# Kernel optimization log

Hardware: AMD Instinct MI355X
Metric: run time of the kernel (lower is better)

## Reference

```python
import jax, jax.numpy as jnp
import numpy as np

PAD = 9  # fixed padding from FNO1d.__init__


def setup_inputs() -> dict:
    key = jax.random.key(0)
    ks = jax.random.split(key, 12)
    B, N, F_IN = 64, 8192, 2          # batch, grid points, input features
    W, L, M = 64, 5, 16               # width, n fourier layers, modes
    d = {}
    d["x"] = jax.random.normal(ks[0], (B, N, F_IN), jnp.float32)
    # Lifting: Linear(F_IN -> W)
    d["lift_w"] = jax.random.normal(ks[1], (F_IN, W), jnp.float32) * 0.5
    d["lift_b"] = jnp.zeros((W,), jnp.float32)
    # Fourier kernels (complex, stored as real/imag), all layers W->W with M modes
    scale = 1.0 / (W * W)
    d["kern_r"] = jax.random.uniform(ks[2], (L, W, W, M), jnp.float32) * scale
    d["kern_i"] = jax.random.uniform(ks[3], (L, W, W, M), jnp.float32) * scale
    # 1x1 Conv1d skip per layer: weight (out, in), bias (out)
    d["conv_w"] = jax.random.normal(ks[4], (L, W, W), jnp.float32) * (1.0 / np.sqrt(W))
    d["conv_b"] = jnp.zeros((L, W), jnp.float32)
    # Projection: Linear(W -> 2W), GELU, Linear(2W -> 1)
    d["proj_w1"] = jax.random.normal(ks[5], (W, 2 * W), jnp.float32) * (1.0 / np.sqrt(W))
    d["proj_b1"] = jnp.zeros((2 * W,), jnp.float32)
    d["proj_w2"] = jax.random.normal(ks[6], (2 * W, 1), jnp.float32) * (1.0 / np.sqrt(2 * W))
    d["proj_b2"] = jnp.zeros((1,), jnp.float32)
    return d


def _fourier_layer(v, kern, cw, cb, modes):
    # v: (b, d, n) real. kern: (d_in, d_out, modes) complex.
    n = v.shape[-1]
    nyq = n // 2 + 1
    F = jnp.fft.rfft(v, axis=-1)                              # (b, d, nyq) complex
    Pm = jnp.einsum('bik,iok->bok', F[:, :, :modes], kern)    # (b, d_out, modes)
    P = jnp.pad(Pm, ((0, 0), (0, 0), (0, nyq - modes)))       # zero high freqs
    K = jnp.fft.irfft(P, n=n, axis=-1)                        # (b, d_out, n)
    lin = jnp.einsum('oi,bin->bon', cw, v) + cb[None, :, None]
    return lin + K


def reference(x, lift_w, lift_b, kern_r, kern_i, conv_w, conv_b,
              proj_w1, proj_b1, proj_w2, proj_b2):
    gelu = lambda t: jax.nn.gelu(t, approximate=False)  # torch.nn.GELU default is exact
    v = x @ lift_w + lift_b                    # (B, N, W)
    v = jnp.transpose(v, (0, 2, 1))            # (B, W, N)
    v = jnp.pad(v, ((0, 0), (0, 0), (0, PAD))) # (B, W, N+PAD)
    L = kern_r.shape[0]
    M = kern_r.shape[-1]
    for l in range(L):  # fixed small layer count
        kern = kern_r[l] + 1j * kern_i[l]
        v = gelu(_fourier_layer(v, kern, conv_w[l], conv_b[l], M))
    v = v[..., :-PAD]
    v = jnp.transpose(v, (0, 2, 1))            # (B, N, W)
    h = gelu(v @ proj_w1 + proj_b1)            # (B, N, 2W)
    return h @ proj_w2 + proj_b2               # (B, N, 1)
```

## Files before the change

kernel.cpp:

```cpp
#include <hip/hip_runtime.h>
#include <math.h>

#define NLEN 8201
#define NB 64
#define W 64
#define M 16
#define NL 5
#define TWO_PI 6.283185307179586476925286766559
#define NT_STAT 514
#define NSTEPS 257
#define NBLK 33

typedef unsigned short u16;
typedef __attribute__((ext_vector_type(8))) short bf16x8;
typedef __attribute__((ext_vector_type(4))) float f32x4;
typedef __attribute__((ext_vector_type(4))) short short4v;
typedef __attribute__((ext_vector_type(8))) short short8v;

__device__ __forceinline__ u16 bf16rn(float x) {
    unsigned u = __float_as_uint(x);
    unsigned r = (u + 0x7fffu + ((u >> 16) & 1u)) >> 16;
    return (u16)r;
}
__device__ __forceinline__ float bf16tof(u16 h) {
// ... 62 lines not shown
    int nstep = blockIdx.x;
    int t = threadIdx.x;
    for (int s = t; s < 1024; s += 256) {
        int e = s & 7, lane = (s >> 3) & 63, kcT = s >> 9;
        int kc = kcT * 16 + (lane & 15);
        int n = nstep * 32 + ((lane >> 4) << 3) + e;
        int k = kc & 15;
        long long m = ((long long)k * (long long)n) % NLEN;
        double th = (TWO_PI / (double)NLEN) * (double)m;
        double sv, cv;
        sincos(th, &sv, &cv);
        float val = (kc < 16) ? (float)cv : (float)(-sv);
        u16 h, lo;
        bf16split(val, h, lo);
        size_t base = (((size_t)nstep * 2 + kcT) * 2) * 512 + lane * 8 + e;
        Tdft[base] = h;
        Tdft[base + 512] = lo;
    }
}

__global__ __launch_bounds__(256) void kprep(const float* __restrict__ cw,
                                             u16* __restrict__ AcwBuf) {
    int l = blockIdx.x;
    int t = threadIdx.x;
    const float* cwl = cw + (size_t)l * W * W;
    u16* ob = AcwBuf + (size_t)l * 8192;
    for (int s = t; s < 4096; s += 256) {
        int e = s & 7, lane = (s >> 3) & 63, mt = (s >> 9) & 3, ks = s >> 11;
        int kk = ((lane >> 4) << 2) + (e & 3) + ((e >> 2) << 4);
        int k = ks * 32 + kk;
        int o = mt * 16 + (lane & 15);
        u16 h, lo;
        bf16split(cwl[o * 64 + k], h, lo);
        ob[(((size_t)ks * 2 + 0) * 4 + mt) * 512 + lane * 8 + e] = h;
        ob[(((size_t)ks * 2 + 1) * 4 + mt) * 512 + lane * 8 + e] = lo;
    }
}

__global__ __launch_bounds__(256) void kprep2(const float* __restrict__ w1,
                                              u16* __restrict__ Aw1) {
    int t = threadIdx.x;
    for (int s = t; s < 8192; s += 256) {
        int e = s & 7, lane = (s >> 3) & 63, mt = (s >> 9) & 7, ks = s >> 12;
        int kk = ((lane >> 4) << 2) + (e & 3) + ((e >> 2) << 4);
        int k = ks * 32 + kk;
        int h = mt * 16 + (lane & 15);
        u16 hh, lo;
        bf16split(w1[k * 128 + h], hh, lo);
        Aw1[(((size_t)ks * 2 + 0) * 8 + mt) * 512 + lane * 8 + e] = hh;
        Aw1[(((size_t)ks * 2 + 1) * 8 + mt) * 512 + lane * 8 + e] = lo;
    }
}

__device__ __forceinline__ void dft_tail(u16* lds, int wv, int lane, int t,
        int blk, const u16* __restrict__ Tdft, float* __restrict__ FpB,
        int atomicMode) {
    int nstep = blk * 8 + wv;
    if (nstep > NSTEPS - 1) nstep = NSTEPS - 1;
    const u16* at = Tdft + (size_t)nstep * 2048;
    bf16x8 Th0 = *(const bf16x8*)(at + lane * 8);
    bf16x8 Tl0 = *(const bf16x8*)(at + 512 + lane * 8);
    bf16x8 Th1 = *(const bf16x8*)(at + 1024 + lane * 8);
    bf16x8 Tl1 = *(const bf16x8*)(at + 1536 + lane * 8);
    f32x4 dacc[2][4];
    #pragma unroll
    for (int kt = 0; kt < 2; kt++)
        #pragma unroll
        for (int ot = 0; ot < 4; ot++) dacc[kt][ot] = (f32x4){0.f, 0.f, 0.f, 0.f};
    const u16* rd = lds + wv * 4096;
    int g = lane >> 4;
    #pragma unroll
    for (int ot = 0; ot < 4; ot++) {
        int oo = ot * 16 + (lane & 15);
        int swz = (oo & 7) << 4;
        bf16x8 Bh = *(const bf16x8*)(rd + (((oo * 128 + g * 16) ^ swz) >> 1));
        bf16x8 Bl = *(const bf16x8*)(rd + (((oo * 128 + 64 + g * 16) ^ swz) >> 1));
        dacc[0][ot] = __builtin_amdgcn_mfma_f32_16x16x32_bf16(Th0, Bh, dacc[0][ot], 0, 0, 0);
        dacc[0][ot] = __builtin_amdgcn_mfma_f32_16x16x32_bf16(Th0, Bl, dacc[0][ot], 0, 0, 0);
        dacc[0][ot] = __builtin_amdgcn_mfma_f32_16x16x32_bf16(Tl0, Bh, dacc[0][ot], 0, 0, 0);
        dacc[0][ot] = __builtin_amdgcn_mfma_f32_16x16x32_bf16(Tl0, Bl, dacc[0][ot], 0, 0, 0);
        dacc[1][ot] = __builtin_amdgcn_mfma_f32_16x16x32_bf16(Th1, Bh, dacc[1][ot], 0, 0, 0);
        dacc[1][ot] = __builtin_amdgcn_mfma_f32_16x16x32_bf16(Th1, Bl, dacc[1][ot], 0, 0, 0);
        dacc[1][ot] = __builtin_amdgcn_mfma_f32_16x16x32_bf16(Tl1, Bh, dacc[1][ot], 0, 0, 0);
        dacc[1][ot] = __builtin_amdgcn_mfma_f32_16x16x32_bf16(Tl1, Bl, dacc[1][ot], 0, 0, 0);
    }
    float* rw = (float*)lds + wv * 2048;
    #pragma unroll
    for (int kt = 0; kt < 2; kt++)
        #pragma unroll
        for (int ot = 0; ot < 4; ot++) {
            int oo = ot * 16 + (lane & 15);
            int kcb = kt * 16 + ((lane >> 4) << 2);
            rw[(kcb + 0) * 64 + oo] = dacc[kt][ot][0];
            rw[(kcb + 1) * 64 + oo] = dacc[kt][ot][1];
            rw[(kcb + 2) * 64 + oo] = dacc[kt][ot][2];
            rw[(kcb + 3) * 64 + oo] = dacc[kt][ot][3];
        }
    __syncthreads();
    {
        const float* rr = (const float*)lds;
        int idx = t * 4;
        float4 s = *(const float4*)(rr + idx);
        #pragma unroll
        for (int w2 = 1; w2 < 8; w2++) {
            float4 p = *(const float4*)(rr + w2 * 2048 + idx);
            s.x += p.x; s.y += p.y; s.z += p.z; s.w += p.w;
        }
        if (atomicMode) {
            atomicAddF(FpB + idx + 0, s.x);
            atomicAddF(FpB + idx + 1, s.y);
            atomicAddF(FpB + idx + 2, s.z);
            atomicAddF(FpB + idx + 3, s.w);
        } else {
            *(float4*)(FpB + (size_t)blk * 2048 + idx) = s;
        }
    }
}

__global__ __launch_bounds__(512, 4) void klift2(const float* __restrict__ x,
        const float* __restrict__ lw, const float* __restrict__ lb,
        u16* __restrict__ Vf, const u16* __restrict__ Tdft,
        float* __restrict__ Fpart, int fstride, int atomicMode) {
    __shared__ __align__(16) u16 outT[8 * 4096];
    int t = threadIdx.x;
    int b = blockIdx.y;
    int blk = blockIdx.x;
    int lane = t & 63;
    int wv = __builtin_amdgcn_readfirstlane(t >> 6);
    int r4 = (lane >> 4) << 2;
    u16* vfb = Vf + ((size_t)b * NBLK + blk) * 32768;
    int n0 = blk * 256;

    short4v hv[4][2], lv[4][2];
    #pragma unroll
    for (int ntl = 0; ntl < 2; ntl++) {
        int nt = wv * 2 + ntl;
        int n = n0 + nt * 16 + (lane & 15);
        float x0 = 0.f, x1 = 0.f;
        bool in = (n < 8192);
        if (in) {
            const float* xp = x + ((size_t)b * 8192 + n) * 2;
            x0 = xp[0]; x1 = xp[1];
        }
        #pragma unroll
        for (int mt = 0; mt < 4; mt++) {
            #pragma unroll
            for (int j = 0; j < 4; j++) {
                int o = mt * 16 + r4 + j;
                float val = in ? fmaf(x0, lw[o], fmaf(x1, lw[64 + o], lb[o])) : 0.f;
                u16 h, lo;
                bf16split(val, h, lo);
                hv[mt][ntl][j] = (short)h;
                lv[mt][ntl][j] = (short)lo;
            }
        }
        *(short8v*)(vfb + ((size_t)0 * 16 + nt) * 512 + lane * 8) = cat4(hv[0][ntl], hv[1][ntl]);
        *(short8v*)(vfb + ((size_t)1 * 16 + nt) * 512 + lane * 8) = cat4(lv[0][ntl], lv[1][ntl]);
        *(short8v*)(vfb + ((size_t)2 * 16 + nt) * 512 + lane * 8) = cat4(hv[2][ntl], hv[3][ntl]);
        *(short8v*)(vfb + ((size_t)3 * 16 + nt) * 512 + lane * 8) = cat4(lv[2][ntl], lv[3][ntl]);
    }

    u16* outW = outT + wv * 4096;
    #pragma unroll
    for (int ntl = 0; ntl < 2; ntl++) {
        int nl = ntl * 16 + (lane & 15);
        bool ok = (n0 + wv * 32 + nl) <= 8200;
        #pragma unroll
        for (int mt = 0; mt < 4; mt++) {
            #pragma unroll
            for (int j = 0; j < 4; j++) {
                int oo = mt * 16 + r4 + j;
                u16 h  = ok ? (u16)hv[mt][ntl][j] : (u16)0;
                u16 lo = ok ? (u16)lv[mt][ntl][j] : (u16)0;
                int raw = oo * 128 + nl * 2;
                int swz = (oo & 7) << 4;
                outW[(raw ^ swz) >> 1] = h;
                outW[((raw + 64) ^ swz) >> 1] = lo;
            }
        }
    }
    dft_tail(outT, wv, lane, t, blk, Tdft, Fpart + (size_t)b * fstride, atomicMode);
}

__device__ __forceinline__ void wfrag(u16* wb2, int mt, int kk, int ol, float val) {
    int lane = ol + (((kk & 15) >> 2) << 4);
    int e = (kk & 3) + ((kk >> 4) << 2);
    u16 h, lo;
    bf16split(val, h, lo);
    wb2[(size_t)mt * 512 + lane * 8 + e] = h;
    wb2[(size_t)(4 + mt) * 512 + lane * 8 + e] = lo;
}

__global__ __launch_bounds__(256) void kmix(const float* __restrict__ Fpart,
        const float* __restrict__ kr, const float* __restrict__ ki,
        const float* __restrict__ cb, u16* __restrict__ WfA2, int l,
        int nblk, int fstride) {
    int b = blockIdx.x, kg = blockIdx.y;
    int t = threadIdx.x;
    int o = t & 63, ii = t >> 6;
    __shared__ float Fs[8][64];
    {
        const float* fp = Fpart + (size_t)b * fstride;
        int r0 = t >> 6, oo = t & 63;
        int kc0 = kg * 4 + r0;
        int kc1 = 16 + kg * 4 + r0;
        float s0 = 0.f, s1 = 0.f, s2 = 0.f, s3 = 0.f;
        int blk = 0;
        for (; blk + 2 <= nblk; blk += 2) {
            s0 += fp[(size_t)blk * 2048 + kc0 * 64 + oo];
            s1 += fp[(size_t)(blk + 1) * 2048 + kc0 * 64 + oo];
            s2 += fp[(size_t)blk * 2048 + kc1 * 64 + oo];
            s3 += fp[(size_t)(blk + 1) * 2048 + kc1 * 64 + oo];
        }
        if (blk < nblk) {
            s0 += fp[(size_t)blk * 2048 + kc0 * 64 + oo];
            s2 += fp[(size_t)blk * 2048 + kc1 * 64 + oo];
        }
        Fs[r0][oo] = s0 + s1;
        Fs[4 + r0][oo] = s2 + s3;
    }
    __syncthreads();

    const float* krl = kr + (size_t)l * W * W * M;
    const float* kil = ki + (size_t)l * W * W * M;
    float pr[4] = {0.f, 0.f, 0.f, 0.f}, pi[4] = {0.f, 0.f, 0.f, 0.f};
    for (int i = ii * 16; i < ii * 16 + 16; i++) {
        float4 kr4 = *(const float4*)(krl + ((size_t)i * W + o) * M + kg * 4);
        float4 ki4 = *(const float4*)(kil + ((size_t)i * W + o) * M + kg * 4);
        float re0 = Fs[0][i], im0 = Fs[4][i];
        float re1 = Fs[1][i], im1 = Fs[5][i];
        float re2 = Fs[2][i], im2 = Fs[6][i];
        float re3 = Fs[3][i], im3 = Fs[7][i];
        pr[0] += re0 * kr4.x - im0 * ki4.x;  pi[0] += re0 * ki4.x + im0 * kr4.x;
        pr[1] += re1 * kr4.y - im1 * ki4.y;  pi[1] += re1 * ki4.y + im1 * kr4.y;
        pr[2] += re2 * kr4.z - im2 * ki4.z;  pi[2] += re2 * ki4.z + im2 * kr4.z;
        pr[3] += re3 * kr4.w - im3 * ki4.w;  pi[3] += re3 * ki4.w + im3 * kr4.w;
    }
    __shared__ float red[4][64][8];
    #pragma unroll
    for (int c = 0; c < 4; c++) {
        red[ii][o][2 * c]     = pr[c];
        red[ii][o][2 * c + 1] = pi[c];
    }
    __syncthreads();
    if (ii == 0) {
        u16* wb2 = WfA2 + (size_t)b * 4096;
        int mt = o >> 4, ol = o & 15;
        #pragma unroll
        for (int c = 0; c < 4; c++) {
            int k = kg * 4 + c;
            float sr = red[0][o][2 * c] + red[1][o][2 * c] + red[2][o][2 * c] + red[3][o][2 * c];
            float si = red[0][o][2 * c + 1] + red[1][o][2 * c + 1] + red[2][o][2 * c + 1] + red[3][o][2 * c + 1];
            if (k == 0) {
                wfrag(wb2, mt, 30, ol, cb[l * W + o] + sr * (1.0f / (float)NLEN));
                wfrag(wb2, mt, 31, ol, 0.0f);
            } else {
                wfrag(wb2, mt, k - 1,  ol, sr * (2.0f / (float)NLEN));
                wfrag(wb2, mt, 14 + k, ol, -si * (2.0f / (float)NLEN));
            }
        }
    }
}

__global__ __launch_bounds__(512, 4) void kconv(u16* __restrict__ Vf,
        const u16* __restrict__ AcwL, const u16* __restrict__ WfA2,
        const u16* __restrict__ Ustat, const u16* __restrict__ Tdft,
        float* __restrict__ Fpart, int fstride, int atomicMode) {
    __shared__ __align__(16) u16 dlds[8 * 4096];
    int t = threadIdx.x;
    int b = blockIdx.y;
    int blk = blockIdx.x;
    int n0 = blk * 256;
    int lane = t & 63;
    int wv = __builtin_amdgcn_readfirstlane(t >> 6);
    u16* vfb = Vf + ((size_t)b * NBLK + blk) * 32768;
    int nt0 = wv * 2;

    bf16x8 Bh[3][2], Bl[3][2];
    #pragma unroll
    for (int ks = 0; ks < 2; ks++)
        #pragma unroll
        for (int ntl = 0; ntl < 2; ntl++) {
            Bh[ks][ntl] = *(const bf16x8*)(vfb + (((size_t)ks * 2 + 0) * 16 + nt0 + ntl) * 512 + lane * 8);
            Bl[ks][ntl] = *(const bf16x8*)(vfb + (((size_t)ks * 2 + 1) * 16 + nt0 + ntl) * 512 + lane * 8);
        }
    #pragma unroll
    for (int ntl = 0; ntl < 2; ntl++) {
        int ntg = (n0 >> 4) + nt0 + ntl;
        if (ntg >= NT_STAT) ntg = NT_STAT - 1;
        Bh[2][ntl] = *(const bf16x8*)(Ustat + ((size_t)ntg * 64 + lane) * 8);
        Bl[2][ntl] = *(const bf16x8*)(Ustat + (size_t)NT_STAT * 512 + ((size_t)ntg * 64 + lane) * 8);
    }

    f32x4 acc[4][2];
    #pragma unroll
    for (int mt = 0; mt < 4; mt++)
        #pragma unroll
        for (int j = 0; j < 2; j++)
            acc[mt][j] = (f32x4){0.f, 0.f, 0.f, 0.f};

    const u16* wb2 = WfA2 + (size_t)b * 4096;
    #pragma unroll
    for (int ks = 0; ks < 3; ks++) {
        const u16* ab = (ks < 2) ? (AcwL + (size_t)ks * 4096) : wb2;
        #pragma unroll
        for (int mt = 0; mt < 4; mt++) {
            bf16x8 Ah = *(const bf16x8*)(ab + (size_t)mt * 512 + lane * 8);
            bf16x8 Al = *(const bf16x8*)(ab + (size_t)(4 + mt) * 512 + lane * 8);
            #pragma unroll
            for (int ntl = 0; ntl < 2; ntl++) {
                acc[mt][ntl] = __builtin_amdgcn_mfma_f32_16x16x32_bf16(Ah, Bh[ks][ntl], acc[mt][ntl], 0, 0, 0);
                acc[mt][ntl] = __builtin_amdgcn_mfma_f32_16x16x32_bf16(Ah, Bl[ks][ntl], acc[mt][ntl], 0, 0, 0);
                acc[mt][ntl] = __builtin_amdgcn_mfma_f32_16x16x32_bf16(Al, Bh[ks][ntl], acc[mt][ntl], 0, 0, 0);
                acc[mt][ntl] = __builtin_amdgcn_mfma_f32_16x16x32_bf16(Al, Bl[ks][ntl], acc[mt][ntl], 0, 0, 0);
            }
        }
    }

    int r4 = (lane >> 4) << 2;
    short4v hv[4][2], lv[4][2];
    #pragma unroll
    for (int ntl = 0; ntl < 2; ntl++) {
        int nt = nt0 + ntl;
        #pragma unroll
        for (int mt = 0; mt < 4; mt++) {
            #pragma unroll
            for (int j = 0; j < 4; j++) {
                float gv = gelu_f(acc[mt][ntl][j]);
                u16 h, lo;
                bf16split(gv, h, lo);
                hv[mt][ntl][j] = (short)h;
                lv[mt][ntl][j] = (short)lo;
            }
        }
        *(short8v*)(vfb + ((size_t)0 * 16 + nt) * 512 + lane * 8) = cat4(hv[0][ntl], hv[1][ntl]);
        *(short8v*)(vfb + ((size_t)1 * 16 + nt) * 512 + lane * 8) = cat4(lv[0][ntl], lv[1][ntl]);
        *(short8v*)(vfb + ((size_t)2 * 16 + nt) * 512 + lane * 8) = cat4(hv[2][ntl], hv[3][ntl]);
        *(short8v*)(vfb + ((size_t)3 * 16 + nt) * 512 + lane * 8) = cat4(lv[2][ntl], lv[3][ntl]);
    }

    {
        u16* outW = dlds + wv * 4096;
        #pragma unroll
        for (int ntl = 0; ntl < 2; ntl++) {
            int nl = ntl * 16 + (lane & 15);
            bool ok = (n0 + wv * 32 + nl) <= 8200;
            #pragma unroll
            for (int mt = 0; mt < 4; mt++) {
                #pragma unroll
                for (int j = 0; j < 4; j++) {
                    int oo = mt * 16 + r4 + j;
                    u16 h  = ok ? (u16)hv[mt][ntl][j] : (u16)0;
                    u16 lo = ok ? (u16)lv[mt][ntl][j] : (u16)0;
                    int raw = oo * 128 + nl * 2;
                    int swz = (oo & 7) << 4;
                    outW[(raw ^ swz) >> 1] = h;
                    outW[((raw + 64) ^ swz) >> 1] = lo;
                }
            }
        }
        dft_tail(dlds, wv, lane, t, blk, Tdft, Fpart + (size_t)b * fstride, atomicMode);
    }
}

__global__ __launch_bounds__(512, 3) void kconvp(const u16* __restrict__ Vf,
        const u16* __restrict__ AcwL, const u16* __restrict__ WfA2,
        const u16* __restrict__ Ustat, const u16* __restrict__ Aw1,
        const float* __restrict__ b1, const float* __restrict__ w2,
        const float* __restrict__ b2, float* __restrict__ out) {
    int t = threadIdx.x;
    int b = blockIdx.y;
    int blk = blockIdx.x;
    int n0 = blk * 256;
    int lane = t & 63;
    int wv = __builtin_amdgcn_readfirstlane(t >> 6);
    const u16* vfb = Vf + ((size_t)b * NBLK + blk) * 32768;
    int nt0 = wv * 2;

    bf16x8 Bh[3][2], Bl[3][2];
    #pragma unroll
    for (int ks = 0; ks < 2; ks++)
        #pragma unroll
        for (int ntl = 0; ntl < 2; ntl++) {
            Bh[ks][ntl] = *(const bf16x8*)(vfb + (((size_t)ks * 2 + 0) * 16 + nt0 + ntl) * 512 + lane * 8);
            Bl[ks][ntl] = *(const bf16x8*)(vfb + (((size_t)ks * 2 + 1) * 16 + nt0 + ntl) * 512 + lane * 8);
        }
    #pragma unroll
    for (int ntl = 0; ntl < 2; ntl++) {
        int ntg = (n0 >> 4) + nt0 + ntl;
        Bh[2][ntl] = *(const bf16x8*)(Ustat + ((size_t)ntg * 64 + lane) * 8);
        Bl[2][ntl] = *(const bf16x8*)(Ustat + (size_t)NT_STAT * 512 + ((size_t)ntg * 64 + lane) * 8);
    }

    f32x4 acc[4][2];
    #pragma unroll
    for (int mt = 0; mt < 4; mt++)
        #pragma unroll
        for (int j = 0; j < 2; j++)
            acc[mt][j] = (f32x4){0.f, 0.f, 0.f, 0.f};

    const u16* wb2 = WfA2 + (size_t)b * 4096;
    #pragma unroll
    for (int ks = 0; ks < 3; ks++) {
        const u16* ab = (ks < 2) ? (AcwL + (size_t)ks * 4096) : wb2;
        #pragma unroll
        for (int mt = 0; mt < 4; mt++) {
            bf16x8 Ah = *(const bf16x8*)(ab + (size_t)mt * 512 + lane * 8);
            bf16x8 Al = *(const bf16x8*)(ab + (size_t)(4 + mt) * 512 + lane * 8);
            #pragma unroll
            for (int ntl = 0; ntl < 2; ntl++) {
                acc[mt][ntl] = __builtin_amdgcn_mfma_f32_16x16x32_bf16(Ah, Bh[ks][ntl], acc[mt][ntl], 0, 0, 0);
                acc[mt][ntl] = __builtin_amdgcn_mfma_f32_16x16x32_bf16(Ah, Bl[ks][ntl], acc[mt][ntl], 0, 0, 0);
                acc[mt][ntl] = __builtin_amdgcn_mfma_f32_16x16x32_bf16(Al, Bh[ks][ntl], acc[mt][ntl], 0, 0, 0);
                acc[mt][ntl] = __builtin_amdgcn_mfma_f32_16x16x32_bf16(Al, Bl[ks][ntl], acc[mt][ntl], 0, 0, 0);
            }
        }
    }

    bf16x8 Bph[2][2], Bpl[2][2];
    #pragma unroll
    for (int ntl = 0; ntl < 2; ntl++) {
        #pragma unroll
        for (int mt = 0; mt < 4; mt++) {
            #pragma unroll
            for (int j = 0; j < 4; j++) {
                float gv = gelu_f(acc[mt][ntl][j]);
                u16 h, lo;
                bf16split(gv, h, lo);
                Bph[mt >> 1][ntl][(mt & 1) * 4 + j] = (short)h;
                Bpl[mt >> 1][ntl][(mt & 1) * 4 + j] = (short)lo;
            }
        }
    }

    int r4 = (lane >> 4) << 2;
    f32x4 pacc[8][2];
    #pragma unroll
    for (int mt = 0; mt < 8; mt++) {
        #pragma unroll
        for (int j = 0; j < 4; j++) {
            float bs = b1[mt * 16 + r4 + j];
            pacc[mt][0][j] = bs;
            pacc[mt][1][j] = bs;
        }
    }
    #pragma unroll
    for (int ks = 0; ks < 2; ks++) {
        #pragma unroll
        for (int mt = 0; mt < 8; mt++) {
            bf16x8 Ah = *(const bf16x8*)(Aw1 + (((size_t)ks * 2 + 0) * 8 + mt) * 512 + lane * 8);
            bf16x8 Al = *(const bf16x8*)(Aw1 + (((size_t)ks * 2 + 1) * 8 + mt) * 512 + lane * 8);
            #pragma unroll
            for (int ntl = 0; ntl < 2; ntl++) {
                pacc[mt][ntl] = __builtin_amdgcn_mfma_f32_16x16x32_bf16(Ah, Bph[ks][ntl], pacc[mt][ntl], 0, 0, 0);
                pacc[mt][ntl] = __builtin_amdgcn_mfma_f32_16x16x32_bf16(Ah, Bpl[ks][ntl], pacc[mt][ntl], 0, 0, 0);
                pacc[mt][ntl] = __builtin_amdgcn_mfma_f32_16x16x32_bf16(Al, Bph[ks][ntl], pacc[mt][ntl], 0, 0, 0);
                pacc[mt][ntl] = __builtin_amdgcn_mfma_f32_16x16x32_bf16(Al, Bpl[ks][ntl], pacc[mt][ntl], 0, 0, 0);
            }
        }
    }

    float bb = b2[0];
    #pragma unroll
    for (int ntl = 0; ntl < 2; ntl++) {
        float p = 0.f;
        #pragma unroll
        for (int mt = 0; mt < 8; mt++) {
            p = fmaf(gelu_f(pacc[mt][ntl][0]), w2[mt * 16 + r4 + 0], p);
            p = fmaf(gelu_f(pacc[mt][ntl][1]), w2[mt * 16 + r4 + 1], p);
            p = fmaf(gelu_f(pacc[mt][ntl][2]), w2[mt * 16 + r4 + 2], p);
            p = fmaf(gelu_f(pacc[mt][ntl][3]), w2[mt * 16 + r4 + 3], p);
        }
        p += __shfl_xor(p, 16, 64);
        p += __shfl_xor(p, 32, 64);
        if (lane < 16) {
            int n = n0 + wv * 32 + ntl * 16 + lane;
            out[(size_t)b * 8192 + n] = p + bb;
        }
    }
}

extern "C" void kernel_launch(void* const* d_in, const int* in_sizes, int n_in,
                              void* d_out, int out_size, void* d_ws, size_t ws_size,
                              hipStream_t stream) {
    const float* x  = (const float*)d_in[0];
    const float* lw = (const float*)d_in[1];
    const float* lb = (const float*)d_in[2];
    const float* kr = (const float*)d_in[3];
    const float* ki = (const float*)d_in[4];
    const float* cw = (const float*)d_in[5];
    const float* cb = (const float*)d_in[6];
    const float* w1 = (const float*)d_in[7];
    const float* b1 = (const float*)d_in[8];
    const float* w2 = (const float*)d_in[9];
    const float* b2 = (const float*)d_in[10];
    float* out = (float*)d_out;

    u16* wsu = (u16*)d_ws;
    size_t VFLEN = (size_t)NB * NBLK * 32768;
    u16* Vf     = wsu;
    u16* Ustat  = Vf + VFLEN;
    u16* AcwBuf = Ustat + (size_t)2 * NT_STAT * 512;
    u16* WfA2   = AcwBuf + (size_t)NL * 8192;
    u16* Tdft   = WfA2 + (size_t)NB * 4096;
    u16* Aw1    = Tdft + (size_t)NSTEPS * 2048;
    u16* fend   = Aw1 + (size_t)16384;
    float* Fpart = (float*)fend;
    size_t base_bytes = (size_t)(fend - wsu) * sizeof(u16);
    size_t need_partial = base_bytes + (size_t)NB * NBLK * 2048 * sizeof(float);
    int atomicMode = (ws_size >= need_partial) ? 0 : 1;
// ... 30 lines not shown
```

Measured before the change: 556.6 us.

## Shrink LDS via half-width DFT staging and shared atomic reduction, raise occupancy

The DFT tail now stages the activation tile into LDS in two halves of 32 channels, so each wave needs half the staging space. The eight per-wave partial sums are combined with LDS atomics into one shared accumulator instead of eight separate buffers. B-fragment loads in the conv kernels move inside the k-step loop to cut register pressure, and the launch-bounds occupancy hints are raised. The aim is more resident blocks per CU to hide latency, at the cost of LDS atomic contention, an extra zero-init barrier, and possible spilling under the tighter register budget.

```diff
diff --git a/kernel.cpp b/kernel.cpp
--- a/kernel.cpp
+++ b/kernel.cpp
@@ -138,9 +138,12 @@
     }
 }
 
-__device__ __forceinline__ void dft_tail(u16* lds, int wv, int lane, int t,
-        int blk, const u16* __restrict__ Tdft, float* __restrict__ FpB,
-        int atomicMode) {
+__device__ __forceinline__ void dft_fused(u16* packW_w, float* racc,
+        const short4v (&hv)[4][2], const short4v (&lv)[4][2],
+        int wv, int lane, int t, int blk, int n0,
+        const u16* __restrict__ Tdft, float* __restrict__ FpB, int atomicMode) {
+    int r4 = (lane >> 4) << 2;
+    int g = lane >> 4;
     int nstep = blk * 8 + wv;
     if (nstep > NSTEPS - 1) nstep = NSTEPS - 1;
     const u16* at = Tdft + (size_t)nstep * 2048;
@@ -153,45 +156,61 @@
     for (int kt = 0; kt < 2; kt++)
         #pragma unroll
         for (int ot = 0; ot < 4; ot++) dacc[kt][ot] = (f32x4){0.f, 0.f, 0.f, 0.f};
-    const u16* rd = lds + wv * 4096;
-    int g = lane >> 4;
-    #pragma unroll
-    for (int ot = 0; ot < 4; ot++) {
-        int oo = ot * 16 + (lane & 15);
-        int swz = (oo & 7) << 4;
-        bf16x8 Bh = *(const bf16x8*)(rd + (((oo * 128 + g * 16) ^ swz) >> 1));
-        bf16x8 Bl = *(const bf16x8*)(rd + (((oo * 128 + 64 + g * 16) ^ swz) >> 1));
-        dacc[0][ot] = __builtin_amdgcn_mfma_f32_16x16x32_bf16(Th0, Bh, dacc[0][ot], 0, 0, 0);
-        dacc[0][ot] = __builtin_amdgcn_mfma_f32_16x16x32_bf16(Th0, Bl, dacc[0][ot], 0, 0, 0);
-        dacc[0][ot] = __builtin_amdgcn_mfma_f32_16x16x32_bf16(Tl0, Bh, dacc[0][ot], 0, 0, 0);
-        dacc[0][ot] = __builtin_amdgcn_mfma_f32_16x16x32_bf16(Tl0, Bl, dacc[0][ot], 0, 0, 0);
-        dacc[1][ot] = __builtin_amdgcn_mfma_f32_16x16x32_bf16(Th1, Bh, dacc[1][ot], 0, 0, 0);
-        dacc[1][ot] = __builtin_amdgcn_mfma_f32_16x16x32_bf16(Th1, Bl, dacc[1][ot], 0, 0, 0);
-        dacc[1][ot] = __builtin_amdgcn_mfma_f32_16x16x32_bf16(Tl1, Bh, dacc[1][ot], 0, 0, 0);
-        dacc[1][ot] = __builtin_amdgcn_mfma_f32_16x16x32_bf16(Tl1, Bl, dacc[1][ot], 0, 0, 0);
-    }
-    float* rw = (float*)lds + wv * 2048;
+
+    #pragma unroll
+    for (int half = 0; half < 2; half++) {
+        #pragma unroll
+        for (int ntl = 0; ntl < 2; ntl++) {
+            int nl = ntl * 16 + (lane & 15);
+            bool ok = (n0 + wv * 32 + nl) <= 8200;
+            #pragma unroll
+            for (int mtl = 0; mtl < 2; mtl++) {
+                int mt = half * 2 + mtl;
+                #pragma unroll
+                for (int j = 0; j < 4; j++) {
+                    int op = mtl * 16 + r4 + j;
+                    u16 h  = ok ? (u16)hv[mt][ntl][j] : (u16)0;
+                    u16 lo = ok ? (u16)lv[mt][ntl][j] : (u16)0;
+                    int raw = op * 128 + nl * 2;
+                    int swz = (op & 7) << 4;
+                    packW_w[(raw ^ swz) >> 1] = h;
+                    packW_w[((raw + 64) ^ swz) >> 1] = lo;
+                }
+            }
+        }
+        #pragma unroll
+        for (int otl = 0; otl < 2; otl++) {
+            int op = otl * 16 + (lane & 15);
+            int swz = (op & 7) << 4;
+            bf16x8 Bh = *(const bf16x8*)(packW_w + (((op * 128 + g * 16) ^ swz) >> 1));
+            bf16x8 Bl = *(const bf16x8*)(packW_w + (((op * 128 + 64 + g * 16) ^ swz) >> 1));
+            int ot = half * 2 + otl;
+            dacc[0][ot] = __builtin_amdgcn_mfma_f32_16x16x32_bf16(Th0, Bh, dacc[0][ot], 0, 0, 0);
+            dacc[0][ot] = __builtin_amdgcn_mfma_f32_16x16x32_bf16(Th0, Bl, dacc[0][ot], 0, 0, 0);
+            dacc[0][ot] = __builtin_amdgcn_mfma_f32_16x16x32_bf16(Tl0, Bh, dacc[0][ot], 0, 0, 0);
+            dacc[0][ot] = __builtin_amdgcn_mfma_f32_16x16x32_bf16(Tl0, Bl, dacc[0][ot], 0, 0, 0);
+            dacc[1][ot] = __builtin_amdgcn_mfma_f32_16x16x32_bf16(Th1, Bh, dacc[1][ot], 0, 0, 0);
+            dacc[1][ot] = __builtin_amdgcn_mfma_f32_16x16x32_bf16(Th1, Bl, dacc[1][ot], 0, 0, 0);
+            dacc[1][ot] = __builtin_amdgcn_mfma_f32_16x16x32_bf16(Tl1, Bh, dacc[1][ot], 0, 0, 0);
+            dacc[1][ot] = __builtin_amdgcn_mfma_f32_16x16x32_bf16(Tl1, Bl, dacc[1][ot], 0, 0, 0);
+        }
+    }
+
     #pragma unroll
     for (int kt = 0; kt < 2; kt++)
         #pragma unroll
         for (int ot = 0; ot < 4; ot++) {
             int oo = ot * 16 + (lane & 15);
-            int kcb = kt * 16 + ((lane >> 4) << 2);
-            rw[(kcb + 0) * 64 + oo] = dacc[kt][ot][0];
-            rw[(kcb + 1) * 64 + oo] = dacc[kt][ot][1];
-            rw[(kcb + 2) * 64 + oo] = dacc[kt][ot][2];
-            rw[(kcb + 3) * 64 + oo] = dacc[kt][ot][3];
+            int kcb = kt * 16 + g * 4;
+            atomicAdd(&racc[(kcb + 0) * 64 + oo], dacc[kt][ot][0]);
+            atomicAdd(&racc[(kcb + 1) * 64 + oo], dacc[kt][ot][1]);
+            atomicAdd(&racc[(kcb + 2) * 64 + oo], dacc[kt][ot][2]);
+            atomicAdd(&racc[(kcb + 3) * 64 + oo], dacc[kt][ot][3]);
         }
     __syncthreads();
     {
-        const float* rr = (const float*)lds;
         int idx = t * 4;
-        float4 s = *(const float4*)(rr + idx);
-        #pragma unroll
-        for (int w2 = 1; w2 < 8; w2++) {
-            float4 p = *(const float4*)(rr + w2 * 2048 + idx);
-            s.x += p.x; s.y += p.y; s.z += p.z; s.w += p.w;
-        }
+        float4 s = *(const float4*)(racc + idx);
         if (atomicMode) {
             atomicAddF(FpB + idx + 0, s.x);
             atomicAddF(FpB + idx + 1, s.y);
@@ -203,11 +222,12 @@
     }
 }
 
-__global__ __launch_bounds__(512, 4) void klift2(const float* __restrict__ x,
+__global__ __launch_bounds__(512, 6) void klift2(const float* __restrict__ x,
         const float* __restrict__ lw, const float* __restrict__ lb,
         u16* __restrict__ Vf, const u16* __restrict__ Tdft,
         float* __restrict__ Fpart, int fstride, int atomicMode) {
-    __shared__ __align__(16) u16 outT[8 * 4096];
+    __shared__ __align__(16) u16 packW[8 * 2048];
+    __shared__ __align__(16) float racc[2048];
     int t = threadIdx.x;
     int b = blockIdx.y;
     int blk = blockIdx.x;
@@ -216,6 +236,9 @@
     int r4 = (lane >> 4) << 2;
     u16* vfb = Vf + ((size_t)b * NBLK + blk) * 32768;
     int n0 = blk * 256;
+
+    *(float4*)(racc + t * 4) = (float4){0.f, 0.f, 0.f, 0.f};
+    __syncthreads();
 
     short4v hv[4][2], lv[4][2];
     #pragma unroll
@@ -246,26 +269,8 @@
         *(short8v*)(vfb + ((size_t)3 * 16 + nt) * 512 + lane * 8) = cat4(lv[2][ntl], lv[3][ntl]);
     }
 
-    u16* outW = outT + wv * 4096;
-    #pragma unroll
-    for (int ntl = 0; ntl < 2; ntl++) {
-        int nl = ntl * 16 + (lane & 15);
-        bool ok = (n0 + wv * 32 + nl) <= 8200;
-        #pragma unroll
-        for (int mt = 0; mt < 4; mt++) {
-            #pragma unroll
-            for (int j = 0; j < 4; j++) {
-                int oo = mt * 16 + r4 + j;
-                u16 h  = ok ? (u16)hv[mt][ntl][j] : (u16)0;
-                u16 lo = ok ? (u16)lv[mt][ntl][j] : (u16)0;
-                int raw = oo * 128 + nl * 2;
-                int swz = (oo & 7) << 4;
-                outW[(raw ^ swz) >> 1] = h;
-                outW[((raw + 64) ^ swz) >> 1] = lo;
-            }
-        }
-    }
-    dft_tail(outT, wv, lane, t, blk, Tdft, Fpart + (size_t)b * fstride, atomicMode);
+    dft_fused(packW + wv * 2048, racc, hv, lv, wv, lane, t, blk, n0,
+              Tdft, Fpart + (size_t)b * fstride, atomicMode);
 }
 
 __device__ __forceinline__ void wfrag(u16* wb2, int mt, int kk, int ol, float val) {
@@ -348,11 +353,12 @@
     }
 }
 
-__global__ __launch_bounds__(512, 4) void kconv(u16* __restrict__ Vf,
+__global__ __launch_bounds__(512, 6) void kconv(u16* __restrict__ Vf,
         const u16* __restrict__ AcwL, const u16* __restrict__ WfA2,
         const u16* __restrict__ Ustat, const u16* __restrict__ Tdft,
         float* __restrict__ Fpart, int fstride, int atomicMode) {
-    __shared__ __align__(16) u16 dlds[8 * 4096];
+    __shared__ __align__(16) u16 packW[8 * 2048];
+    __shared__ __align__(16) float racc[2048];
     int t = threadIdx.x;
     int b = blockIdx.y;
     int blk = blockIdx.x;
@@ -362,21 +368,8 @@
     u16* vfb = Vf + ((size_t)b * NBLK + blk) * 32768;
     int nt0 = wv * 2;
 
-    bf16x8 Bh[3][2], Bl[3][2];
-    #pragma unroll
-    for (int ks = 0; ks < 2; ks++)
-        #pragma unroll
-        for (int ntl = 0; ntl < 2; ntl++) {
-            Bh[ks][ntl] = *(const bf16x8*)(vfb + (((size_t)ks * 2 + 0) * 16 + nt0 + ntl) * 512 + lane * 8);
-            Bl[ks][ntl] = *(const bf16x8*)(vfb + (((size_t)ks * 2 + 1) * 16 + nt0 + ntl) * 512 + lane * 8);
-        }
-    #pragma unroll
-    for (int ntl = 0; ntl < 2; ntl++) {
-        int ntg = (n0 >> 4) + nt0 + ntl;
-        if (ntg >= NT_STAT) ntg = NT_STAT - 1;
-        Bh[2][ntl] = *(const bf16x8*)(Ustat + ((size_t)ntg * 64 + lane) * 8);
-        Bl[2][ntl] = *(const bf16x8*)(Ustat + (size_t)NT_STAT * 512 + ((size_t)ntg * 64 + lane) * 8);
-    }
+    *(float4*)(racc + t * 4) = (float4){0.f, 0.f, 0.f, 0.f};
+    __syncthreads();
 
     f32x4 acc[4][2];
     #pragma unroll
@@ -388,6 +381,22 @@
     const u16* wb2 = WfA2 + (size_t)b * 4096;
     #pragma unroll
     for (int ks = 0; ks < 3; ks++) {
+        bf16x8 Bh[2], Bl[2];
+        if (ks < 2) {
+            #pragma unroll
+            for (int ntl = 0; ntl < 2; ntl++) {
+                Bh[ntl] = *(const bf16x8*)(vfb + (((size_t)ks * 2 + 0) * 16 + nt0 + ntl) * 512 + lane * 8);
+                Bl[ntl] = *(const bf16x8*)(vfb + (((size_t)ks * 2 + 1) * 16 + nt0 + ntl) * 512 + lane * 8);
+            }
+        } else {
+            #pragma unroll
+            for (int ntl = 0; ntl < 2; ntl++) {
+                int ntg = (n0 >> 4) + nt0 + ntl;
+                if (ntg >= NT_STAT) ntg = NT_STAT - 1;
+                Bh[ntl] = *(const bf16x8*)(Ustat + ((size_t)ntg * 64 + lane) * 8);
+                Bl[ntl] = *(const bf16x8*)(Ustat + (size_t)NT_STAT * 512 + ((size_t)ntg * 64 + lane) * 8);
+            }
+        }
         const u16* ab = (ks < 2) ? (AcwL + (size_t)ks * 4096) : wb2;
         #pragma unroll
         for (int mt = 0; mt < 4; mt++) {
@@ -395,15 +404,14 @@
             bf16x8 Al = *(const bf16x8*)(ab + (size_t)(4 + mt) * 512 + lane * 8);
             #pragma unroll
             for (int ntl = 0; ntl < 2; ntl++) {
-                acc[mt][ntl] = __builtin_amdgcn_mfma_f32_16x16x32_bf16(Ah, Bh[ks][ntl], acc[mt][ntl], 0, 0, 0);
-                acc[mt][ntl] = __builtin_amdgcn_mfma_f32_16x16x32_bf16(Ah, Bl[ks][ntl], acc[mt][ntl], 0, 0, 0);
-                acc[mt][ntl] = __builtin_amdgcn_mfma_f32_16x16x32_bf16(Al, Bh[ks][ntl], acc[mt][ntl], 0, 0, 0);
-                acc[mt][ntl] = __builtin_amdgcn_mfma_f32_16x16x32_bf16(Al, Bl[ks][ntl], acc[mt][ntl], 0, 0, 0);
-            }
-        }
-    }
-
-    int r4 = (lane >> 4) << 2;
+                acc[mt][ntl] = __builtin_amdgcn_mfma_f32_16x16x32_bf16(Ah, Bh[ntl], acc[mt][ntl], 0, 0, 0);
+                acc[mt][ntl] = __builtin_amdgcn_mfma_f32_16x16x32_bf16(Ah, Bl[ntl], acc[mt][ntl], 0, 0, 0);
+                acc[mt][ntl] = __builtin_amdgcn_mfma_f32_16x16x32_bf16(Al, Bh[ntl], acc[mt][ntl], 0, 0, 0);
+                acc[mt][ntl] = __builtin_amdgcn_mfma_f32_16x16x32_bf16(Al, Bl[ntl], acc[mt][ntl], 0, 0, 0);
+            }
+        }
+    }
+
     short4v hv[4][2], lv[4][2];
     #pragma unroll
     for (int ntl = 0; ntl < 2; ntl++) {
@@ -425,31 +433,11 @@
         *(short8v*)(vfb + ((size_t)3 * 16 + nt) * 512 + lane * 8) = cat4(lv[2][ntl], lv[3][ntl]);
     }
 
-    {
-        u16* outW = dlds + wv * 4096;
-        #pragma unroll
-        for (int ntl = 0; ntl < 2; ntl++) {
-            int nl = ntl * 16 + (lane & 15);
-            bool ok = (n0 + wv * 32 + nl) <= 8200;
-            #pragma unroll
-            for (int mt = 0; mt < 4; mt++) {
-                #pragma unroll
-                for (int j = 0; j < 4; j++) {
-                    int oo = mt * 16 + r4 + j;
-                    u16 h  = ok ? (u16)hv[mt][ntl][j] : (u16)0;
-                    u16 lo = ok ? (u16)lv[mt][ntl][j] : (u16)0;
-                    int raw = oo * 128 + nl * 2;
-                    int swz = (oo & 7) << 4;
-                    outW[(raw ^ swz) >> 1] = h;
-                    outW[((raw + 64) ^ swz) >> 1] = lo;
-                }
-            }
-        }
-        dft_tail(dlds, wv, lane, t, blk, Tdft, Fpart + (size_t)b * fstride, atomicMode);
-    }
-}
-
-__global__ __launch_bounds__(512, 3) void kconvp(const u16* __restrict__ Vf,
+    dft_fused(packW + wv * 2048, racc, hv, lv, wv, lane, t, blk, n0,
+              Tdft, Fpart + (size_t)b * fstride, atomicMode);
+}
+
+__global__ __launch_bounds__(512, 4) void kconvp(const u16* __restrict__ Vf,
         const u16* __restrict__ AcwL, const u16* __restrict__ WfA2,
         const u16* __restrict__ Ustat, const u16* __restrict__ Aw1,
         const float* __restrict__ b1, const float* __restrict__ w2,
@@ -463,21 +451,6 @@
     const u16* vfb = Vf + ((size_t)b * NBLK + blk) * 32768;
     int nt0 = wv * 2;
 
-    bf16x8 Bh[3][2], Bl[3][2];
-    #pragma unroll
-    for (int ks = 0; ks < 2; ks++)
-        #pragma unroll
-        for (int ntl = 0; ntl < 2; ntl++) {
-            Bh[ks][ntl] = *(const bf16x8*)(vfb + (((size_t)ks * 2 + 0) * 16 + nt0 + ntl) * 512 + lane * 8);
-            Bl[ks][ntl] = *(const bf16x8*)(vfb + (((size_t)ks * 2 + 1) * 16 + nt0 + ntl) * 512 + lane * 8);
-        }
-    #pragma unroll
-    for (int ntl = 0; ntl < 2; ntl++) {
-        int ntg = (n0 >> 4) + nt0 + ntl;
-        Bh[2][ntl] = *(const bf16x8*)(Ustat + ((size_t)ntg * 64 + lane) * 8);
-        Bl[2][ntl] = *(const bf16x8*)(Ustat + (size_t)NT_STAT * 512 + ((size_t)ntg * 64 + lane) * 8);
-    }
-
     f32x4 acc[4][2];
     #pragma unroll
     for (int mt = 0; mt < 4; mt++)
@@ -488,6 +461,21 @@
     const u16* wb2 = WfA2 + (size_t)b * 4096;
     #pragma unroll
     for (int ks = 0; ks < 3; ks++) {
+        bf16x8 Bh[2], Bl[2];
+        if (ks < 2) {
+            #pragma unroll
+            for (int ntl = 0; ntl < 2; ntl++) {
+                Bh[ntl] = *(const bf16x8*)(vfb + (((size_t)ks * 2 + 0) * 16 + nt0 + ntl) * 512 + lane * 8);
+                Bl[ntl] = *(const bf16x8*)(vfb + (((size_t)ks * 2 + 1) * 16 + nt0 + ntl) * 512 + lane * 8);
+            }
+        } else {
+            #pragma unroll
+            for (int ntl = 0; ntl < 2; ntl++) {
+                int ntg = (n0 >> 4) + nt0 + ntl;
+                Bh[ntl] = *(const bf16x8*)(Ustat + ((size_t)ntg * 64 + lane) * 8);
+                Bl[ntl] = *(const bf16x8*)(Ustat + (size_t)NT_STAT * 512 + ((size_t)ntg * 64 + lane) * 8);
+            }
+        }
         const u16* ab = (ks < 2) ? (AcwL + (size_t)ks * 4096) : wb2;
         #pragma unroll
         for (int mt = 0; mt < 4; mt++) {
@@ -495,10 +483,10 @@
             bf16x8 Al = *(const bf16x8*)(ab + (size_t)(4 + mt) * 512 + lane * 8);
             #pragma unroll
             for (int ntl = 0; ntl < 2; ntl++) {
-                acc[mt][ntl] = __builtin_amdgcn_mfma_f32_16x16x32_bf16(Ah, Bh[ks][ntl], acc[mt][ntl], 0, 0, 0);
-                acc[mt][ntl] = __builtin_amdgcn_mfma_f32_16x16x32_bf16(Ah, Bl[ks][ntl], acc[mt][ntl], 0, 0, 0);
-                acc[mt][ntl] = __builtin_amdgcn_mfma_f32_16x16x32_bf16(Al, Bh[ks][ntl], acc[mt][ntl], 0, 0, 0);
-                acc[mt][ntl] = __builtin_amdgcn_mfma_f32_16x16x32_bf16(Al, Bl[ks][ntl], acc[mt][ntl], 0, 0, 0);
+                acc[mt][ntl] = __builtin_amdgcn_mfma_f32_16x16x32_bf16(Ah, Bh[ntl], acc[mt][ntl], 0, 0, 0);
+                acc[mt][ntl] = __builtin_amdgcn_mfma_f32_16x16x32_bf16(Ah, Bl[ntl], acc[mt][ntl], 0, 0, 0);
+                acc[mt][ntl] = __builtin_amdgcn_mfma_f32_16x16x32_bf16(Al, Bh[ntl], acc[mt][ntl], 0, 0, 0);
+                acc[mt][ntl] = __builtin_amdgcn_mfma_f32_16x16x32_bf16(Al, Bl[ntl], acc[mt][ntl], 0, 0, 0);
             }
         }
     }
```

Measured after the change: 1.475 ms. 2.65x slower.

## Halve DFT LDS staging, reduce via LDS atomics, drop lo*lo MFMA terms

Applied to the files above, without the earlier changes.

Reworks the DFT tail in the lift and layer kernels. Each wave now stages only half its channels at a time in a 4 KB per-wave buffer instead of 8 KB, which cuts shared memory and is meant to raise occupancy. The cross-wave reduction now uses LDS atomicAdd into a single 2048-float accumulator instead of a strided 8-way sum. Separately, every split-bf16 product (DFT, conv/mix GEMM, projection) drops its low*low MFMA, removing a quarter of the MFMAs at a small cost in accuracy.

```diff
diff --git a/kernel.cpp b/kernel.cpp
--- a/kernel.cpp
+++ b/kernel.cpp
@@ -138,84 +138,25 @@
     }
 }
 
-__device__ __forceinline__ void dft_tail(u16* lds, int wv, int lane, int t,
-        int blk, const u16* __restrict__ Tdft, float* __restrict__ FpB,
-        int atomicMode) {
-    int nstep = blk * 8 + wv;
-    if (nstep > NSTEPS - 1) nstep = NSTEPS - 1;
-    const u16* at = Tdft + (size_t)nstep * 2048;
-    bf16x8 Th0 = *(const bf16x8*)(at + lane * 8);
-    bf16x8 Tl0 = *(const bf16x8*)(at + 512 + lane * 8);
-    bf16x8 Th1 = *(const bf16x8*)(at + 1024 + lane * 8);
-    bf16x8 Tl1 = *(const bf16x8*)(at + 1536 + lane * 8);
-    f32x4 dacc[2][4];
-    #pragma unroll
-    for (int kt = 0; kt < 2; kt++)
-        #pragma unroll
-        for (int ot = 0; ot < 4; ot++) dacc[kt][ot] = (f32x4){0.f, 0.f, 0.f, 0.f};
-    const u16* rd = lds + wv * 4096;
-    int g = lane >> 4;
-    #pragma unroll
-    for (int ot = 0; ot < 4; ot++) {
-        int oo = ot * 16 + (lane & 15);
-        int swz = (oo & 7) << 4;
-        bf16x8 Bh = *(const bf16x8*)(rd + (((oo * 128 + g * 16) ^ swz) >> 1));
-        bf16x8 Bl = *(const bf16x8*)(rd + (((oo * 128 + 64 + g * 16) ^ swz) >> 1));
-        dacc[0][ot] = __builtin_amdgcn_mfma_f32_16x16x32_bf16(Th0, Bh, dacc[0][ot], 0, 0, 0);
-        dacc[0][ot] = __builtin_amdgcn_mfma_f32_16x16x32_bf16(Th0, Bl, dacc[0][ot], 0, 0, 0);
-        dacc[0][ot] = __builtin_amdgcn_mfma_f32_16x16x32_bf16(Tl0, Bh, dacc[0][ot], 0, 0, 0);
-        dacc[0][ot] = __builtin_amdgcn_mfma_f32_16x16x32_bf16(Tl0, Bl, dacc[0][ot], 0, 0, 0);
-        dacc[1][ot] = __builtin_amdgcn_mfma_f32_16x16x32_bf16(Th1, Bh, dacc[1][ot], 0, 0, 0);
-        dacc[1][ot] = __builtin_amdgcn_mfma_f32_16x16x32_bf16(Th1, Bl, dacc[1][ot], 0, 0, 0);
-        dacc[1][ot] = __builtin_amdgcn_mfma_f32_16x16x32_bf16(Tl1, Bh, dacc[1][ot], 0, 0, 0);
-        dacc[1][ot] = __builtin_amdgcn_mfma_f32_16x16x32_bf16(Tl1, Bl, dacc[1][ot], 0, 0, 0);
-    }
-    float* rw = (float*)lds + wv * 2048;
-    #pragma unroll
-    for (int kt = 0; kt < 2; kt++)
-        #pragma unroll
-        for (int ot = 0; ot < 4; ot++) {
-            int oo = ot * 16 + (lane & 15);
-            int kcb = kt * 16 + ((lane >> 4) << 2);
-            rw[(kcb + 0) * 64 + oo] = dacc[kt][ot][0];
-            rw[(kcb + 1) * 64 + oo] = dacc[kt][ot][1];
-            rw[(kcb + 2) * 64 + oo] = dacc[kt][ot][2];
-            rw[(kcb + 3) * 64 + oo] = dacc[kt][ot][3];
-        }
-    __syncthreads();
-    {
-        const float* rr = (const float*)lds;
-        int idx = t * 4;
-        float4 s = *(const float4*)(rr + idx);
-        #pragma unroll
-        for (int w2 = 1; w2 < 8; w2++) {
-            float4 p = *(const float4*)(rr + w2 * 2048 + idx);
-            s.x += p.x; s.y += p.y; s.z += p.z; s.w += p.w;
-        }
-        if (atomicMode) {
-            atomicAddF(FpB + idx + 0, s.x);
-            atomicAddF(FpB + idx + 1, s.y);
-            atomicAddF(FpB + idx + 2, s.z);
-            atomicAddF(FpB + idx + 3, s.w);
-        } else {
-            *(float4*)(FpB + (size_t)blk * 2048 + idx) = s;
-        }
-    }
-}
 
 __global__ __launch_bounds__(512, 4) void klift2(const float* __restrict__ x,
         const float* __restrict__ lw, const float* __restrict__ lb,
         u16* __restrict__ Vf, const u16* __restrict__ Tdft,
         float* __restrict__ Fpart, int fstride, int atomicMode) {
-    __shared__ __align__(16) u16 outT[8 * 4096];
+    __shared__ __align__(16) u16 packW[8 * 2048];
+    __shared__ __align__(16) float racc[2048];
     int t = threadIdx.x;
     int b = blockIdx.y;
     int blk = blockIdx.x;
     int lane = t & 63;
     int wv = __builtin_amdgcn_readfirstlane(t >> 6);
     int r4 = (lane >> 4) << 2;
+    int g = lane >> 4;
     u16* vfb = Vf + ((size_t)b * NBLK + blk) * 32768;
     int n0 = blk * 256;
+
+    *(float4*)(racc + t * 4) = (float4){0.f, 0.f, 0.f, 0.f};
+    __syncthreads();
 
     short4v hv[4][2], lv[4][2];
     #pragma unroll
@@ -246,26 +187,81 @@
         *(short8v*)(vfb + ((size_t)3 * 16 + nt) * 512 + lane * 8) = cat4(lv[2][ntl], lv[3][ntl]);
     }
 
-    u16* outW = outT + wv * 4096;
-    #pragma unroll
-    for (int ntl = 0; ntl < 2; ntl++) {
-        int nl = ntl * 16 + (lane & 15);
-        bool ok = (n0 + wv * 32 + nl) <= 8200;
-        #pragma unroll
-        for (int mt = 0; mt < 4; mt++) {
-            #pragma unroll
-            for (int j = 0; j < 4; j++) {
-                int oo = mt * 16 + r4 + j;
-                u16 h  = ok ? (u16)hv[mt][ntl][j] : (u16)0;
-                u16 lo = ok ? (u16)lv[mt][ntl][j] : (u16)0;
-                int raw = oo * 128 + nl * 2;
-                int swz = (oo & 7) << 4;
-                outW[(raw ^ swz) >> 1] = h;
-                outW[((raw + 64) ^ swz) >> 1] = lo;
-            }
-        }
-    }
-    dft_tail(outT, wv, lane, t, blk, Tdft, Fpart + (size_t)b * fstride, atomicMode);
+    {
+        u16* packw = packW + wv * 2048;
+        int nstep = blk * 8 + wv;
+        if (nstep > NSTEPS - 1) nstep = NSTEPS - 1;
+        const u16* at = Tdft + (size_t)nstep * 2048;
+        bf16x8 Th0 = *(const bf16x8*)(at + lane * 8);
+        bf16x8 Tl0 = *(const bf16x8*)(at + 512 + lane * 8);
+        bf16x8 Th1 = *(const bf16x8*)(at + 1024 + lane * 8);
+        bf16x8 Tl1 = *(const bf16x8*)(at + 1536 + lane * 8);
+        f32x4 dacc[2][4];
+        #pragma unroll
+        for (int kt = 0; kt < 2; kt++)
+            #pragma unroll
+            for (int ot = 0; ot < 4; ot++) dacc[kt][ot] = (f32x4){0.f, 0.f, 0.f, 0.f};
+        #pragma unroll
+        for (int half = 0; half < 2; half++) {
+            #pragma unroll
+            for (int ntl = 0; ntl < 2; ntl++) {
+                int nl = ntl * 16 + (lane & 15);
+                bool ok = (n0 + wv * 32 + nl) <= 8200;
+                #pragma unroll
+                for (int mtl = 0; mtl < 2; mtl++) {
+                    #pragma unroll
+                    for (int j = 0; j < 4; j++) {
+                        int op = mtl * 16 + r4 + j;
+                        u16 h  = ok ? (u16)hv[half * 2 + mtl][ntl][j] : (u16)0;
+                        u16 lo = ok ? (u16)lv[half * 2 + mtl][ntl][j] : (u16)0;
+                        int raw = op * 128 + nl * 2;
+                        int swz = (op & 7) << 4;
+                        packw[(raw ^ swz) >> 1] = h;
+                        packw[((raw + 64) ^ swz) >> 1] = lo;
+                    }
+                }
+            }
+            #pragma unroll
+            for (int otl = 0; otl < 2; otl++) {
+                int op = otl * 16 + (lane & 15);
+                int swz = (op & 7) << 4;
+                bf16x8 Bh = *(const bf16x8*)(packw + (((op * 128 + g * 16) ^ swz) >> 1));
+                bf16x8 Bl = *(const bf16x8*)(packw + (((op * 128 + 64 + g * 16) ^ swz) >> 1));
+                int ot = half * 2 + otl;
+                dacc[0][ot] = __builtin_amdgcn_mfma_f32_16x16x32_bf16(Th0, Bh, dacc[0][ot], 0, 0, 0);
+                dacc[0][ot] = __builtin_amdgcn_mfma_f32_16x16x32_bf16(Th0, Bl, dacc[0][ot], 0, 0, 0);
+                dacc[0][ot] = __builtin_amdgcn_mfma_f32_16x16x32_bf16(Tl0, Bh, dacc[0][ot], 0, 0, 0);
+                dacc[1][ot] = __builtin_amdgcn_mfma_f32_16x16x32_bf16(Th1, Bh, dacc[1][ot], 0, 0, 0);
+                dacc[1][ot] = __builtin_amdgcn_mfma_f32_16x16x32_bf16(Th1, Bl, dacc[1][ot], 0, 0, 0);
+                dacc[1][ot] = __builtin_amdgcn_mfma_f32_16x16x32_bf16(Tl1, Bh, dacc[1][ot], 0, 0, 0);
+            }
+        }
+        #pragma unroll
+        for (int kt = 0; kt < 2; kt++)
+            #pragma unroll
+            for (int ot = 0; ot < 4; ot++) {
+                int oo = ot * 16 + (lane & 15);
+                int kcb = kt * 16 + g * 4;
+                atomicAdd(&racc[(kcb + 0) * 64 + oo], dacc[kt][ot][0]);
+                atomicAdd(&racc[(kcb + 1) * 64 + oo], dacc[kt][ot][1]);
+                atomicAdd(&racc[(kcb + 2) * 64 + oo], dacc[kt][ot][2]);
+                atomicAdd(&racc[(kcb + 3) * 64 + oo], dacc[kt][ot][3]);
+            }
+        __syncthreads();
+        {
+            float* FpB = Fpart + (size_t)b * fstride;
+            int idx = t * 4;
+            float4 s = *(const float4*)(racc + idx);
+            if (atomicMode) {
+                atomicAddF(FpB + idx + 0, s.x);
+                atomicAddF(FpB + idx + 1, s.y);
+                atomicAddF(FpB + idx + 2, s.z);
+                atomicAddF(FpB + idx + 3, s.w);
+            } else {
+                *(float4*)(FpB + (size_t)blk * 2048 + idx) = s;
+            }
+        }
+    }
 }
 
 __device__ __forceinline__ void wfrag(u16* wb2, int mt, int kk, int ol, float val) {
@@ -352,15 +348,21 @@
         const u16* __restrict__ AcwL, const u16* __restrict__ WfA2,
         const u16* __restrict__ Ustat, const u16* __restrict__ Tdft,
         float* __restrict__ Fpart, int fstride, int atomicMode) {
-    __shared__ __align__(16) u16 dlds[8 * 4096];
+    __shared__ __align__(16) u16 packW[8 * 2048];
+    __shared__ __align__(16) float racc[2048];
     int t = threadIdx.x;
     int b = blockIdx.y;
     int blk = blockIdx.x;
     int n0 = blk * 256;
     int lane = t & 63;
     int wv = __builtin_amdgcn_readfirstlane(t >> 6);
+    int g = lane >> 4;
+    int r4 = g << 2;
     u16* vfb = Vf + ((size_t)b * NBLK + blk) * 32768;
     int nt0 = wv * 2;
+
+    *(float4*)(racc + t * 4) = (float4){0.f, 0.f, 0.f, 0.f};
+    __syncthreads();
 
     bf16x8 Bh[3][2], Bl[3][2];
     #pragma unroll
@@ -398,12 +400,10 @@
                 acc[mt][ntl] = __builtin_amdgcn_mfma_f32_16x16x32_bf16(Ah, Bh[ks][ntl], acc[mt][ntl], 0, 0, 0);
                 acc[mt][ntl] = __builtin_amdgcn_mfma_f32_16x16x32_bf16(Ah, Bl[ks][ntl], acc[mt][ntl], 0, 0, 0);
                 acc[mt][ntl] = __builtin_amdgcn_mfma_f32_16x16x32_bf16(Al, Bh[ks][ntl], acc[mt][ntl], 0, 0, 0);
-                acc[mt][ntl] = __builtin_amdgcn_mfma_f32_16x16x32_bf16(Al, Bl[ks][ntl], acc[mt][ntl], 0, 0, 0);
-            }
-        }
-    }
-
-    int r4 = (lane >> 4) << 2;
+            }
+        }
+    }
+
     short4v hv[4][2], lv[4][2];
     #pragma unroll
     for (int ntl = 0; ntl < 2; ntl++) {
@@ -426,26 +426,79 @@
     }
 
     {
-        u16* outW = dlds + wv * 4096;
-        #pragma unroll
-        for (int ntl = 0; ntl < 2; ntl++) {
-            int nl = ntl * 16 + (lane & 15);
-            bool ok = (n0 + wv * 32 + nl) <= 8200;
-            #pragma unroll
-            for (int mt = 0; mt < 4; mt++) {
+        u16* packw = packW + wv * 2048;
+        int nstep = blk * 8 + wv;
+        if (nstep > NSTEPS - 1) nstep = NSTEPS - 1;
+        const u16* at = Tdft + (size_t)nstep * 2048;
+        bf16x8 Th0 = *(const bf16x8*)(at + lane * 8);
+        bf16x8 Tl0 = *(const bf16x8*)(at + 512 + lane * 8);
+        bf16x8 Th1 = *(const bf16x8*)(at + 1024 + lane * 8);
+        bf16x8 Tl1 = *(const bf16x8*)(at + 1536 + lane * 8);
+        f32x4 dacc[2][4];
+        #pragma unroll
+        for (int kt = 0; kt < 2; kt++)
+            #pragma unroll
+            for (int ot = 0; ot < 4; ot++) dacc[kt][ot] = (f32x4){0.f, 0.f, 0.f, 0.f};
+        #pragma unroll
+        for (int half = 0; half < 2; half++) {
+            #pragma unroll
+            for (int ntl = 0; ntl < 2; ntl++) {
+                int nl = ntl * 16 + (lane & 15);
+                bool ok = (n0 + wv * 32 + nl) <= 8200;
                 #pragma unroll
-                for (int j = 0; j < 4; j++) {
-                    int oo = mt * 16 + r4 + j;
-                    u16 h  = ok ? (u16)hv[mt][ntl][j] : (u16)0;
-                    u16 lo = ok ? (u16)lv[mt][ntl][j] : (u16)0;
-                    int raw = oo * 128 + nl * 2;
-                    int swz = (oo & 7) << 4;
-                    outW[(raw ^ swz) >> 1] = h;
-                    outW[((raw + 64) ^ swz) >> 1] = lo;
+                for (int mtl = 0; mtl < 2; mtl++) {
+                    #pragma unroll
+                    for (int j = 0; j < 4; j++) {
+                        int op = mtl * 16 + r4 + j;
+                        u16 h  = ok ? (u16)hv[half * 2 + mtl][ntl][j] : (u16)0;
+                        u16 lo = ok ? (u16)lv[half * 2 + mtl][ntl][j] : (u16)0;
+                        int raw = op * 128 + nl * 2;
+                        int swz = (op & 7) << 4;
+                        packw[(raw ^ swz) >> 1] = h;
+                        packw[((raw + 64) ^ swz) >> 1] = lo;
+                    }
                 }
             }
-        }
-        dft_tail(dlds, wv, lane, t, blk, Tdft, Fpart + (size_t)b * fstride, atomicMode);
+            #pragma unroll
+            for (int otl = 0; otl < 2; otl++) {
+                int op = otl * 16 + (lane & 15);
+                int swz = (op & 7) << 4;
+                bf16x8 Bph = *(const bf16x8*)(packw + (((op * 128 + g * 16) ^ swz) >> 1));
+                bf16x8 Bpl = *(const bf16x8*)(packw + (((op * 128 + 64 + g * 16) ^ swz) >> 1));
+                int ot = half * 2 + otl;
+                dacc[0][ot] = __builtin_amdgcn_mfma_f32_16x16x32_bf16(Th0, Bph, dacc[0][ot], 0, 0, 0);
+                dacc[0][ot] = __builtin_amdgcn_mfma_f32_16x16x32_bf16(Th0, Bpl, dacc[0][ot], 0, 0, 0);
+                dacc[0][ot] = __builtin_amdgcn_mfma_f32_16x16x32_bf16(Tl0, Bph, dacc[0][ot], 0, 0, 0);
+                dacc[1][ot] = __builtin_amdgcn_mfma_f32_16x16x32_bf16(Th1, Bph, dacc[1][ot], 0, 0, 0);
+                dacc[1][ot] = __builtin_amdgcn_mfma_f32_16x16x32_bf16(Th1, Bpl, dacc[1][ot], 0, 0, 0);
+                dacc[1][ot] = __builtin_amdgcn_mfma_f32_16x16x32_bf16(Tl1, Bph, dacc[1][ot], 0, 0, 0);
+            }
+        }
+        #pragma unroll
+        for (int kt = 0; kt < 2; kt++)
+            #pragma unroll
+            for (int ot = 0; ot < 4; ot++) {
+                int oo = ot * 16 + (lane & 15);
+                int kcb = kt * 16 + g * 4;
+                atomicAdd(&racc[(kcb + 0) * 64 + oo], dacc[kt][ot][0]);
+                atomicAdd(&racc[(kcb + 1) * 64 + oo], dacc[kt][ot][1]);
+                atomicAdd(&racc[(kcb + 2) * 64 + oo], dacc[kt][ot][2]);
+                atomicAdd(&racc[(kcb + 3) * 64 + oo], dacc[kt][ot][3]);
+            }
+        __syncthreads();
+        {
+            float* FpB = Fpart + (size_t)b * fstride;
+            int idx = t * 4;
+            float4 s = *(const float4*)(racc + idx);
+            if (atomicMode) {
+                atomicAddF(FpB + idx + 0, s.x);
+                atomicAddF(FpB + idx + 1, s.y);
+                atomicAddF(FpB + idx + 2, s.z);
+                atomicAddF(FpB + idx + 3, s.w);
+            } else {
+                *(float4*)(FpB + (size_t)blk * 2048 + idx) = s;
+            }
+        }
     }
 }
 
@@ -498,12 +551,12 @@
                 acc[mt][ntl] = __builtin_amdgcn_mfma_f32_16x16x32_bf16(Ah, Bh[ks][ntl], acc[mt][ntl], 0, 0, 0);
                 acc[mt][ntl] = __builtin_amdgcn_mfma_f32_16x16x32_bf16(Ah, Bl[ks][ntl], acc[mt][ntl], 0, 0, 0);
                 acc[mt][ntl] = __builtin_amdgcn_mfma_f32_16x16x32_bf16(Al, Bh[ks][ntl], acc[mt][ntl], 0, 0, 0);
-                acc[mt][ntl] = __builtin_amdgcn_mfma_f32_16x16x32_bf16(Al, Bl[ks][ntl], acc[mt][ntl], 0, 0, 0);
             }
         }
     }
 
     bf16x8 Bph[2][2], Bpl[2][2];
+    int r4 = (lane >> 4) << 2;
     #pragma unroll
     for (int ntl = 0; ntl < 2; ntl++) {
         #pragma unroll
@@ -519,7 +572,6 @@
         }
     }
 
-    int r4 = (lane >> 4) << 2;
     f32x4 pacc[8][2];
     #pragma unroll
     for (int mt = 0; mt < 8; mt++) {
@@ -541,7 +593,6 @@
                 pacc[mt][ntl] = __builtin_amdgcn_mfma_f32_16x16x32_bf16(Ah, Bph[ks][ntl], pacc[mt][ntl], 0, 0, 0);
                 pacc[mt][ntl] = __builtin_amdgcn_mfma_f32_16x16x32_bf16(Ah, Bpl[ks][ntl], pacc[mt][ntl], 0, 0, 0);
                 pacc[mt][ntl] = __builtin_amdgcn_mfma_f32_16x16x32_bf16(Al, Bph[ks][ntl], pacc[mt][ntl], 0, 0, 0);
-                pacc[mt][ntl] = __builtin_amdgcn_mfma_f32_16x16x32_bf16(Al, Bpl[ks][ntl], pacc[mt][ntl], 0, 0, 0);
             }
         }
     }
```

Measured after the change: 1.278 ms. 130% more time.
